# Kernel tuning notes

Measured on AMD Instinct MI355X. Metric: run time of the kernel, lower is better.

Reference implementation:

```python
import jax, jax.numpy as jnp
import numpy as np

N_TYPES = 4
N_PAIRS = N_TYPES * N_TYPES          # 16 (src_type, dst_type) pairs
N_GLOBAL_ET = 24                     # global edge event types
N_LOCAL_ET = 16                      # per-pair predictor output classes
D = 256                              # hidden dim
E = 262144                           # number of edges


def setup_inputs() -> dict:
    key = jax.random.key(0)
    ks = jax.random.split(key, 12)
    s = 0.05
    h_src = jax.random.normal(ks[0], (E, D), jnp.float32)
    h_dst = jax.random.normal(ks[1], (E, D), jnp.float32)
    src_type_idx = jax.random.randint(ks[2], (E,), 0, N_TYPES)
    dst_type_idx = jax.random.randint(ks[3], (E,), 0, N_TYPES)
    edge_type_classes = jax.random.randint(ks[4], (E,), 0, N_GLOBAL_ET)
    # decoder params: Linear(concat(h_src,h_dst)) -> D, split into two matrices
    W1 = jax.random.normal(ks[5], (D, D), jnp.float32) * s
    W2 = jax.random.normal(ks[6], (D, D), jnp.float32) * s
    b_dec = jnp.zeros((D,), jnp.float32)
    # per-(src,dst)-pair predictor heads, stacked
    W_pred = jax.random.normal(ks[7], (N_PAIRS, D, N_LOCAL_ET), jnp.float32) * s
    b_pred = jnp.zeros((N_PAIRS, N_LOCAL_ET), jnp.float32)
    # event_map[pair, global_edge_type] -> local class id
    event_map = jax.random.randint(ks[8], (N_PAIRS, N_GLOBAL_ET), 0, N_LOCAL_ET)
    return {
        'h_src': h_src, 'h_dst': h_dst,
        'W1': W1, 'W2': W2, 'b_dec': b_dec,
        'W_pred': W_pred, 'b_pred': b_pred,
        'src_type_idx': src_type_idx, 'dst_type_idx': dst_type_idx,
        'edge_type_classes': edge_type_classes, 'event_map': event_map,
        'inference': 0,
    }


def reference(h_src, h_dst, W1, W2, b_dec, W_pred, b_pred,
              src_type_idx, dst_type_idx, edge_type_classes, event_map,
              inference):
    # decoder: Linear(concat(h_src, h_dst)) -> D, ReLU
    h = jax.nn.relu(h_src @ W1 + h_dst @ W2 + b_dec)            # [E, D]
    pair = src_type_idx * N_TYPES + dst_type_idx                 # [E]
    # grouped per-pair linear heads: compute all heads, select per-edge head
    logits_all = jnp.einsum('ed,pdc->epc', h, W_pred) + b_pred   # [E, P, C]
    logits = jnp.take_along_axis(
        logits_all, pair[:, None, None], axis=1)[:, 0]           # [E, C]
    labels = event_map[pair, edge_type_classes]                  # [E]
    logp = jax.nn.log_softmax(logits, axis=-1)
    per_edge_loss = -jnp.take_along_axis(logp, labels[:, None], axis=1)[:, 0]
    # training path: per-group mean, then mean over non-empty groups
    sums = jax.ops.segment_sum(per_edge_loss, pair, num_segments=N_PAIRS)
    cnts = jax.ops.segment_sum(jnp.ones_like(per_edge_loss), pair,
                               num_segments=N_PAIRS)
    present = cnts > 0
    gmean = jnp.where(present, sums / jnp.maximum(cnts, 1.0), 0.0)
    loss = jnp.sum(gmean) / jnp.sum(present.astype(jnp.float32))
    return loss
```

## Files before the change

### kernel.cpp

```cpp
#include <hip/hip_runtime.h>
#include <stdint.h>

#define E_EDGES 262144
#define TILE_M 128
#define MAX_TILES 2064

typedef unsigned short ushort_t;
typedef __attribute__((ext_vector_type(8))) short short8;
typedef __attribute__((ext_vector_type(4))) float f32x4;

#define OFF_WT   0
#define OFF_WP   (512*256*2)
#define OFF_PERM (OFF_WP + 16*8*64*8*2)
#define OFF_HIST (OFF_PERM + MAX_TILES*128*4)
#define OFF_SEG  (OFF_HIST + 64)
#define OFF_CUR  (OFF_SEG + 128)
#define OFF_SUMS (OFF_CUR + 64)

__device__ __forceinline__ ushort_t f2bf(float f) {
  union { float f; unsigned u; } c; c.f = f;
  unsigned r = c.u + 0x7fffu + ((c.u >> 16) & 1u);
  return (ushort_t)(r >> 16);
}

__device__ __forceinline__ void async_copy16(void* lds, const void* g) {
  __builtin_amdgcn_global_load_lds(
      (const __attribute__((address_space(1))) unsigned int*)g,
      (__attribute__((address_space(3))) unsigned int*)lds, 16, 0, 0);
}

__global__ __launch_bounds__(256) void prep_k(const float* __restrict__ W1,
    const float* __restrict__ W2, const float* __restrict__ Wp,
    char* __restrict__ ws) {
  const int i = blockIdx.x * 256 + threadIdx.x;
  int* perm = (int*)(ws + OFF_PERM);
  if (i < MAX_TILES * 128) perm[i] = -1;
  if (i < 512 * 256) {
    ushort_t* Wt = (ushort_t*)(ws + OFF_WT);
    const int n = i >> 9, k = i & 511;
    const float v = (k < 256) ? W1[(k << 8) + n] : W2[((k - 256) << 8) + n];
    Wt[i] = f2bf(v);
  }
  if (i < 16 * 8 * 64 * 8) {
    ushort_t* Wpf = (ushort_t*)(ws + OFF_WP);
    const int j = i & 7, l = (i >> 3) & 63, s = (i >> 9) & 7, p = i >> 12;
    const int k = s * 32 + (l >> 4) * 8 + j, c = l & 15;
    Wpf[i] = f2bf(Wp[((p << 8) + k) * 16 + c]);
  }
  if (i < 16) {
    ((int*)(ws + OFF_HIST))[i] = 0;
    ((int*)(ws + OFF_CUR))[i] = 0;
    ((float*)(ws + OFF_SUMS))[i] = 0.f;
  }
}

__global__ __launch_bounds__(256) void hist_k(const int* __restrict__ st,
    const int* __restrict__ dt, char* __restrict__ ws) {
  __shared__ int lh[16];
  int* hist = (int*)(ws + OFF_HIST);
  const int t = threadIdx.x;
  if (t < 16) lh[t] = 0;
  __syncthreads();
  const int i = blockIdx.x * 256 + t;
  if (i < E_EDGES) atomicAdd(&lh[st[i] * 4 + dt[i]], 1);
  __syncthreads();
  if (t < 16 && lh[t] > 0) atomicAdd(&hist[t], lh[t]);
}

__global__ void scan_k(char* __restrict__ ws) {
  if (threadIdx.x == 0) {
    const int* hist = (const int*)(ws + OFF_HIST);
    int* seg = (int*)(ws + OFF_SEG);
    int acc = 0;
    for (int p = 0; p < 16; ++p) {
      seg[p] = acc;
      acc += (hist[p] + 127) & ~127;
    }
    seg[16] = acc;
  }
}

__global__ __launch_bounds__(256) void scatter_k(const int* __restrict__ st,
    const int* __restrict__ dt, char* __restrict__ ws) {
  __shared__ int lh[16], lbase[16];
  const int* seg = (const int*)(ws + OFF_SEG);
  int* cur = (int*)(ws + OFF_CUR);
  int* perm = (int*)(ws + OFF_PERM);
  const int t = threadIdx.x;
  if (t < 16) lh[t] = 0;
  __syncthreads();
  const int i = blockIdx.x * 256 + t;
  int p = 0, r = 0;
  const bool v = (i < E_EDGES);
  if (v) { p = st[i] * 4 + dt[i]; r = atomicAdd(&lh[p], 1); }
  __syncthreads();
  if (t < 16 && lh[t] > 0) lbase[t] = atomicAdd(&cur[t], lh[t]);
  __syncthreads();
  if (v) perm[seg[p] + lbase[p] + r] = i;
}

__global__ __launch_bounds__(512) void main_k(
    const float* __restrict__ h_src, const float* __restrict__ h_dst,
    const float* __restrict__ b_dec, const float* __restrict__ b_pred,
    const int* __restrict__ etc_arr, const int* __restrict__ emap,
    char* __restrict__ ws) {
  const ushort_t* Wt = (const ushort_t*)(ws + OFF_WT);
  const short8* Wpf = (const short8*)(ws + OFF_WP);
  const int* perm = (const int*)(ws + OFF_PERM);
  const int* seg = (const int*)(ws + OFF_SEG);
  float* sums = (float*)(ws + OFF_SUMS);

  const int tb = blockIdx.x * TILE_M;
  if (tb >= seg[16]) return;
  int pair = 0;
#pragma unroll
  for (int p = 1; p < 16; ++p) pair += (tb >= seg[p]) ? 1 : 0;

  __shared__ __align__(16) char smem[65536];
  ushort_t* A_ls = (ushort_t*)smem;
  char* B_ls = smem + 18432;
  ushort_t* H_ls = (ushort_t*)smem;

  const int t = threadIdx.x;
  const int w = t >> 6, lane = t & 63;
  const int quad = lane >> 4, l15 = lane & 15;
  const int wm = w >> 2, wn = w & 3;

  const int arow = t >> 2, acg = t & 3;
  const int e_stage = perm[tb + arow];

  const f32x4 zero4 = {0.f, 0.f, 0.f, 0.f};
  f32x4 acc[4][4];
#pragma unroll
  for (int i = 0; i < 4; ++i)
#pragma unroll
    for (int j = 0; j < 4; ++j) acc[i][j] = zero4;

  for (int kt = 0; kt < 8; ++kt) {
    const float* srcb = (kt < 4) ? h_src : h_dst;
    const int kofs = (kt & 3) * 64 + acg * 16;
    f32x4 fv[4];
    if (e_stage >= 0) {
      const f32x4* gp = (const f32x4*)(srcb + ((size_t)e_stage << 8) + kofs);
#pragma unroll
      for (int q = 0; q < 4; ++q) fv[q] = gp[q];
    } else {
#pragma unroll
      for (int q = 0; q < 4; ++q) fv[q] = zero4;
    }
    union { ushort_t u[16]; short8 v[2]; } pk;
#pragma unroll
    for (int q = 0; q < 4; ++q)
#pragma unroll
      for (int x = 0; x < 4; ++x) pk.u[q * 4 + x] = f2bf(fv[q][x]);
    {
      ushort_t* dst = A_ls + arow * 72 + acg * 16;
      *(short8*)dst = pk.v[0];
      *(short8*)(dst + 8) = pk.v[1];
    }
#pragma unroll
    for (int ci = 0; ci < 4; ++ci) {
      const int chunk = w * 4 + ci;
      const int ks = chunk >> 4, nt = chunk & 15;
      const int n = nt * 16 + l15;
      const int k = kt * 64 + ks * 32 + quad * 8;
      async_copy16(B_ls + chunk * 1024, Wt + n * 512 + k);
    }
    __syncthreads();
#pragma unroll
    for (int ks = 0; ks < 2; ++ks) {
      short8 a[4], b[4];
#pragma unroll
      for (int i = 0; i < 4; ++i)
        a[i] = *(const short8*)(A_ls + (wm * 64 + i * 16 + l15) * 72 + ks * 32 + quad * 8);
#pragma unroll
      for (int j = 0; j < 4; ++j)
        b[j] = *(const short8*)(B_ls + (ks * 16 + wn * 4 + j) * 1024 + lane * 16);
#pragma unroll
      for (int i = 0; i < 4; ++i)
#pragma unroll
        for (int j = 0; j < 4; ++j)
          acc[i][j] = __builtin_amdgcn_mfma_f32_16x16x32_bf16(a[i], b[j], acc[i][j], 0, 0, 0);
    }
    __syncthreads();
  }

  float bj[4];
#pragma unroll
  for (int j = 0; j < 4; ++j) bj[j] = b_dec[wn * 64 + j * 16 + l15];
#pragma unroll
  for (int i = 0; i < 4; ++i)
#pragma unroll
    for (int j = 0; j < 4; ++j)
#pragma unroll
      for (int r = 0; r < 4; ++r) {
        const int row = wm * 64 + i * 16 + quad * 4 + r;
        const int col = wn * 64 + j * 16 + l15;
        float v = acc[i][j][r] + bj[j];
        v = fmaxf(v, 0.f);
        H_ls[row * 256 + col] = f2bf(v);
      }
  __syncthreads();

  f32x4 acc2 = zero4;
#pragma unroll
  for (int s = 0; s < 8; ++s) {
    short8 a = *(const short8*)(H_ls + (w * 16 + l15) * 256 + s * 32 + quad * 8);
    short8 b = Wpf[(pair * 8 + s) * 64 + lane];
    acc2 = __builtin_amdgcn_mfma_f32_16x16x32_bf16(a, b, acc2, 0, 0, 0);
  }

  const float bp = b_pred[pair * 16 + l15];
  float wacc = 0.f;
#pragma unroll
  for (int r = 0; r < 4; ++r) {
    const int row = w * 16 + quad * 4 + r;
    const int e = perm[tb + row];
    float v = acc2[r] + bp;
    float m = v;
#pragma unroll
    for (int o = 1; o < 16; o <<= 1) m = fmaxf(m, __shfl_xor(m, o, 16));
    float sm = __expf(v - m);
#pragma unroll
    for (int o = 1; o < 16; o <<= 1) sm += __shfl_xor(sm, o, 16);
    int label = 0;
    if (e >= 0) label = emap[pair * 24 + etc_arr[e]];
    const float vlab = __shfl(v, (lane & 48) + label, 64);
    if (e >= 0 && l15 == 0) wacc += m + __logf(sm) - vlab;
  }
  wacc += __shfl_xor(wacc, 16, 64);
  wacc += __shfl_xor(wacc, 32, 64);
  if (lane == 0) atomicAdd(&sums[pair], wacc);
}

__global__ void finalize_k(const char* __restrict__ ws, float* __restrict__ out) {
  const float* sums = (const float*)(ws + OFF_SUMS);
  const int* hist = (const int*)(ws + OFF_HIST);
  const int t = threadIdx.x;
  float g = 0.f, pr = 0.f;
  if (t < 16) {
    const int c = hist[t];
    if (c > 0) { g = sums[t] / (float)c; pr = 1.f; }
  }
#pragma unroll
  for (int o = 1; o < 16; o <<= 1) { g += __shfl_xor(g, o, 64); pr += __shfl_xor(pr, o, 64); }
  if (t == 0) out[0] = g / pr;
}

extern "C" void kernel_launch(void* const* d_in, const int* in_sizes, int n_in,
                              void* d_out, int out_size, void* d_ws, size_t ws_size,
                              hipStream_t stream) {
  const float* h_src  = (const float*)d_in[0];
  const float* h_dst  = (const float*)d_in[1];
  const float* W1     = (const float*)d_in[2];
  const float* W2     = (const float*)d_in[3];
  const float* b_dec  = (const float*)d_in[4];
  const float* W_pred = (const float*)d_in[5];
  const float* b_pred = (const float*)d_in[6];
  const int* st   = (const int*)d_in[7];
  const int* dt   = (const int*)d_in[8];
  const int* etc  = (const int*)d_in[9];
  const int* emap = (const int*)d_in[10];
  char* ws = (char*)d_ws;
  float* out = (float*)d_out;

  prep_k<<<(MAX_TILES * 128 + 255) / 256, 256, 0, stream>>>(W1, W2, W_pred, ws);
  hist_k<<<E_EDGES / 256, 256, 0, stream>>>(st, dt, ws);
  scan_k<<<1, 64, 0, stream>>>(ws);
  scatter_k<<<E_EDGES / 256, 256, 0, stream>>>(st, dt, ws);
  main_k<<<MAX_TILES, 512, 0, stream>>>(h_src, h_dst, b_dec, b_pred, etc, emap, ws);
  finalize_k<<<1, 64, 0, stream>>>(ws, out);
}
```

Measured before the change: 721.6 us.

## Software-pipeline the decoder GEMM with double-buffered weights and register-prefetched activations

Restructures the K loop of the main GEMM so activation rows are prefetched two iterations ahead into registers and weight tiles are loaded asynchronously into a double-buffered LDS region. Explicit waitcnt and barrier calls replace the full syncthreads. The A tile uses an XOR swizzle instead of padding, and the H buffer stride is padded to reduce LDS bank conflicts. This is meant to hide global-load latency behind the MFMA work, at the cost of more LDS (80KB, lower occupancy) and more registers, and it relies on hand-written waitcnt counts being correct.

After: 740.7 us. 2.6% more time.

```diff
diff --git a/kernel.cpp b/kernel.cpp
--- a/kernel.cpp
+++ b/kernel.cpp
@@ -16,6 +16,10 @@
 #define OFF_SEG  (OFF_HIST + 64)
 #define OFF_CUR  (OFF_SEG + 128)
 #define OFF_SUMS (OFF_CUR + 64)
+
+#define WAITCNT(vm, lgkm) __builtin_amdgcn_s_waitcnt( \
+    ((vm) & 0xF) | (((vm) & 0x30) << 10) | (0x7 << 4) | (((lgkm) & 0xF) << 8))
+#define SCHED_FENCE() __builtin_amdgcn_sched_barrier(0)
 
 __device__ __forceinline__ ushort_t f2bf(float f) {
   union { float f; unsigned u; } c; c.f = f;
@@ -116,9 +120,10 @@
 #pragma unroll
   for (int p = 1; p < 16; ++p) pair += (tb >= seg[p]) ? 1 : 0;
 
-  __shared__ __align__(16) char smem[65536];
+  __shared__ __align__(16) char smem[81920];
   ushort_t* A_ls = (ushort_t*)smem;
-  char* B_ls = smem + 18432;
+  char* B_ls0 = smem + 16384;
+  char* B_ls1 = smem + 16384 + 32768;
   ushort_t* H_ls = (ushort_t*)smem;
 
   const int t = threadIdx.x;
@@ -128,6 +133,8 @@
 
   const int arow = t >> 2, acg = t & 3;
   const int e_stage = perm[tb + arow];
+  const int e_row = (e_stage >= 0) ? e_stage : 0;
+  const float amask = (e_stage >= 0) ? 1.f : 0.f;
 
   const f32x4 zero4 = {0.f, 0.f, 0.f, 0.f};
   f32x4 acc[4][4];
@@ -136,53 +143,70 @@
 #pragma unroll
     for (int j = 0; j < 4; ++j) acc[i][j] = zero4;
 
-  for (int kt = 0; kt < 8; ++kt) {
+  auto issueA = [&](int kt, f32x4* r) {
     const float* srcb = (kt < 4) ? h_src : h_dst;
-    const int kofs = (kt & 3) * 64 + acg * 16;
-    f32x4 fv[4];
-    if (e_stage >= 0) {
-      const f32x4* gp = (const f32x4*)(srcb + ((size_t)e_stage << 8) + kofs);
-#pragma unroll
-      for (int q = 0; q < 4; ++q) fv[q] = gp[q];
-    } else {
-#pragma unroll
-      for (int q = 0; q < 4; ++q) fv[q] = zero4;
-    }
-    union { ushort_t u[16]; short8 v[2]; } pk;
-#pragma unroll
-    for (int q = 0; q < 4; ++q)
-#pragma unroll
-      for (int x = 0; x < 4; ++x) pk.u[q * 4 + x] = f2bf(fv[q][x]);
-    {
-      ushort_t* dst = A_ls + arow * 72 + acg * 16;
-      *(short8*)dst = pk.v[0];
-      *(short8*)(dst + 8) = pk.v[1];
-    }
+    const f32x4* gp = (const f32x4*)(srcb + ((size_t)e_row << 8) + ((kt & 3) << 6) + (acg << 4));
+#pragma unroll
+    for (int q = 0; q < 4; ++q) r[q] = gp[q];
+  };
+  auto issueB = [&](int kt, char* buf) {
 #pragma unroll
     for (int ci = 0; ci < 4; ++ci) {
       const int chunk = w * 4 + ci;
       const int ks = chunk >> 4, nt = chunk & 15;
       const int n = nt * 16 + l15;
       const int k = kt * 64 + ks * 32 + quad * 8;
-      async_copy16(B_ls + chunk * 1024, Wt + n * 512 + k);
-    }
-    __syncthreads();
-#pragma unroll
-    for (int ks = 0; ks < 2; ++ks) {
-      short8 a[4], b[4];
-#pragma unroll
-      for (int i = 0; i < 4; ++i)
-        a[i] = *(const short8*)(A_ls + (wm * 64 + i * 16 + l15) * 72 + ks * 32 + quad * 8);
-#pragma unroll
-      for (int j = 0; j < 4; ++j)
-        b[j] = *(const short8*)(B_ls + (ks * 16 + wn * 4 + j) * 1024 + lane * 16);
-#pragma unroll
-      for (int i = 0; i < 4; ++i)
+      async_copy16(buf + chunk * 1024, Wt + n * 512 + k);
+    }
+  };
+
+  f32x4 rA[2][4];
+  issueA(0, rA[0]);
+  issueA(1, rA[1]);
+  issueB(0, B_ls0);
+
+#pragma unroll
+  for (int kt = 0; kt < 8; ++kt) {
+    union { ushort_t u[16]; short8 v[2]; } pk;
+#pragma unroll
+    for (int q = 0; q < 4; ++q)
+#pragma unroll
+      for (int x = 0; x < 4; ++x) pk.u[q * 4 + x] = f2bf(rA[kt & 1][q][x] * amask);
+    {
+      ushort_t* rowp = A_ls + arow * 64;
+      *(short8*)(rowp + ((((2 * acg)     ^ (arow & 7)) << 3))) = pk.v[0];
+      *(short8*)(rowp + ((((2 * acg + 1) ^ (arow & 7)) << 3))) = pk.v[1];
+    }
+    if (kt < 7) issueB(kt + 1, (kt & 1) ? B_ls0 : B_ls1);
+    if (kt < 6) issueA(kt + 2, rA[kt & 1]);
+    SCHED_FENCE();
+    if (kt == 7) { WAITCNT(0, 0); } else { WAITCNT(8, 0); }
+    SCHED_FENCE();
+    __builtin_amdgcn_s_barrier();
+    SCHED_FENCE();
+    {
+      const char* Bb = (kt & 1) ? B_ls1 : B_ls0;
+#pragma unroll
+      for (int ks = 0; ks < 2; ++ks) {
+        short8 a[4], b[4];
+#pragma unroll
+        for (int i = 0; i < 4; ++i) {
+          const int row = wm * 64 + i * 16 + l15;
+          a[i] = *(const short8*)(A_ls + row * 64 + ((((ks << 2) | quad) ^ (row & 7)) << 3));
+        }
 #pragma unroll
         for (int j = 0; j < 4; ++j)
-          acc[i][j] = __builtin_amdgcn_mfma_f32_16x16x32_bf16(a[i], b[j], acc[i][j], 0, 0, 0);
-    }
-    __syncthreads();
+          b[j] = *(const short8*)(Bb + (ks * 16 + wn * 4 + j) * 1024 + lane * 16);
+#pragma unroll
+        for (int i = 0; i < 4; ++i)
+#pragma unroll
+          for (int j = 0; j < 4; ++j)
+            acc[i][j] = __builtin_amdgcn_mfma_f32_16x16x32_bf16(a[i], b[j], acc[i][j], 0, 0, 0);
+      }
+    }
+    SCHED_FENCE();
+    __builtin_amdgcn_s_barrier();
+    SCHED_FENCE();
   }
 
   float bj[4];
@@ -198,14 +222,14 @@
         const int col = wn * 64 + j * 16 + l15;
         float v = acc[i][j][r] + bj[j];
         v = fmaxf(v, 0.f);
-        H_ls[row * 256 + col] = f2bf(v);
+        H_ls[row * 264 + col] = f2bf(v);
       }
   __syncthreads();
 
   f32x4 acc2 = zero4;
 #pragma unroll
   for (int s = 0; s < 8; ++s) {
-    short8 a = *(const short8*)(H_ls + (w * 16 + l15) * 256 + s * 32 + quad * 8);
+    short8 a = *(const short8*)(H_ls + (w * 16 + l15) * 264 + s * 32 + quad * 8);
     short8 b = Wpf[(pair * 8 + s) * 64 + lane];
     acc2 = __builtin_amdgcn_mfma_f32_16x16x32_bf16(a, b, acc2, 0, 0, 0);
   }
```
